# Performance work log

Hardware: AMD Instinct MI355X
Metric: run time of the kernel (lower is better)

Reference implementation:

```python
import jax, jax.numpy as jnp
from jax import lax
import numpy as np

C = 56; DI = 112; DS = 16; R = 4; K = 4; NB = 10; UP = 3
B, H, W = 1, 64, 64

def conv2d(x, w, b=None, pad=1, groups=1):
    out = lax.conv_general_dilated(x, w, (1, 1), [(pad, pad), (pad, pad)],
                                   feature_group_count=groups,
                                   dimension_numbers=('NCHW', 'OIHW', 'NCHW'))
    if b is not None:
        out = out + b[None, :, None, None]
    return out

def ln_last(x, w, b, eps=1e-5):
    mu = x.mean(-1, keepdims=True)
    var = ((x - mu) ** 2).mean(-1, keepdims=True)
    return (x - mu) / jnp.sqrt(var + eps) * w + b

def ln_cf(x, w, b, eps=1e-6):
    mu = x.mean(1, keepdims=True)
    var = ((x - mu) ** 2).mean(1, keepdims=True)
    return (x - mu) / jnp.sqrt(var + eps) * w[None, :, None, None] + b[None, :, None, None]

def bsconv(x, pw_w, dw_w, dw_b):
    x = conv2d(x, pw_w, pad=0)
    return conv2d(x, dw_w, dw_b, pad=1, groups=dw_w.shape[0])

def ss2d(x, p):
    # x: (B,H,W,C) -> SS2D (VMamba 4-direction selective scan)
    b, h, w, _ = x.shape
    L = h * w
    xz = x @ p['inproj_w'].T                        # (B,H,W,2*DI)
    xin, z = jnp.split(xz, 2, axis=-1)
    xc = jnp.transpose(xin, (0, 3, 1, 2))           # (B,DI,H,W)
    xc = jax.nn.silu(conv2d(xc, p['conv_w'], p['conv_b'], pad=1, groups=DI))
    xf = xc.reshape(b, DI, L)
    xt = jnp.swapaxes(xc, 2, 3).reshape(b, DI, L)
    x_hwwh = jnp.stack([xf, xt], axis=1)            # (B,2,DI,L)
    xs = jnp.concatenate([x_hwwh, jnp.flip(x_hwwh, -1)], axis=1)  # (B,K,DI,L)
    x_dbl = jnp.einsum('bkdl,kcd->bkcl', xs, p['xproj_w'])
    dts, Bs, Cs = jnp.split(x_dbl, [R, R + DS], axis=2)
    dts = jnp.einsum('bkrl,kdr->bkdl', dts, p['dt_w'])
    A = -jnp.exp(p['Alog'].reshape(K, DI, DS))
    delta = jax.nn.softplus(dts + p['dt_b'][None, :, :, None])    # (B,K,DI,L)

    def step(hst, inp):
        dl, xl, bl, cl = inp
        dA = jnp.exp(dl[..., None] * A[None])       # (B,K,DI,DS)
        hst = dA * hst + (dl * xl)[..., None] * bl[:, :, None, :]
        y = jnp.einsum('bkdn,bkn->bkd', hst, cl)
        return hst, y

    seq = (jnp.transpose(delta, (3, 0, 1, 2)), jnp.transpose(xs, (3, 0, 1, 2)),
           jnp.transpose(Bs, (3, 0, 1, 2)), jnp.transpose(Cs, (3, 0, 1, 2)))
    h0 = jnp.zeros((b, K, DI, DS), x.dtype)
    _, ys = lax.scan(step, h0, seq)                 # (L,B,K,DI)
    out_y = jnp.transpose(ys, (1, 2, 3, 0)) + p['D'].reshape(K, DI)[None, :, :, None] * xs
    inv = jnp.flip(out_y[:, 2:4], -1)
    y1 = out_y[:, 0]
    y2 = inv[:, 0]
    y3 = jnp.swapaxes(inv[:, 1].reshape(b, DI, w, h), 2, 3).reshape(b, DI, L)
    y4 = jnp.swapaxes(out_y[:, 1].reshape(b, DI, w, h), 2, 3).reshape(b, DI, L)
    y = jnp.swapaxes(y1 + y2 + y3 + y4, 1, 2).reshape(b, h, w, DI)
    y = ln_last(y, p['onorm_w'], p['onorm_b'])
    y = y * jax.nn.silu(z)
    return y @ p['outproj_w'].T

def safm(x, mfr_w, mfr_b, aggr_w, aggr_b):
    b, c, h, w = x.shape
    ch = c // 4
    parts = jnp.split(x, 4, axis=1)
    outs = []
    for i in range(4):
        s = parts[i]
        f = 2 ** i
        if i > 0:
            s = s.reshape(b, ch, h // f, f, w // f, f).max(axis=(3, 5))
        s = conv2d(s, mfr_w[i], mfr_b[i], pad=1, groups=ch)
        if i > 0:
            s = jnp.repeat(jnp.repeat(s, f, axis=2), f, axis=3)
        outs.append(s)
    out = conv2d(jnp.concatenate(outs, axis=1), aggr_w, aggr_b, pad=0)
    return jax.nn.gelu(out, approximate=False) * x

def afd(x, p):
    xn = jnp.transpose(x, (0, 2, 3, 1))
    xn = xn + ss2d(ln_last(xn, p['ln1_w'], p['ln1_b']), p)   # VSSBlock residual
    x = jnp.transpose(xn, (0, 3, 1, 2))
    x = x + safm(ln_cf(x, p['norm_w'], p['norm_b']), p['mfr_w'], p['mfr_b'], p['aggr_w'], p['aggr_b'])
    return x, x

def _forward(x, fea_pw_w, fea_dw_w, fea_dw_b,
             blk_ln1_w, blk_ln1_b, blk_inproj_w, blk_conv_w, blk_conv_b,
             blk_xproj_w, blk_dt_w, blk_dt_b, blk_Alog, blk_D,
             blk_onorm_w, blk_onorm_b, blk_outproj_w,
             blk_norm_w, blk_norm_b, blk_mfr_w, blk_mfr_b, blk_aggr_w, blk_aggr_b,
             c1_w, c1_b, norm_w, norm_b, c2_pw_w, c2_dw_w, c2_dw_b, up_w, up_b):
    out_fea = bsconv(x, fea_pw_w, fea_dw_w, fea_dw_b)
    bp = {'ln1_w': blk_ln1_w, 'ln1_b': blk_ln1_b, 'inproj_w': blk_inproj_w,
          'conv_w': blk_conv_w, 'conv_b': blk_conv_b, 'xproj_w': blk_xproj_w,
          'dt_w': blk_dt_w, 'dt_b': blk_dt_b, 'Alog': blk_Alog, 'D': blk_D,
          'onorm_w': blk_onorm_w, 'onorm_b': blk_onorm_b, 'outproj_w': blk_outproj_w,
          'norm_w': blk_norm_w, 'norm_b': blk_norm_b, 'mfr_w': blk_mfr_w,
          'mfr_b': blk_mfr_b, 'aggr_w': blk_aggr_w, 'aggr_b': blk_aggr_b}
    _, outs = lax.scan(afd, out_fea, bp)            # (NB,B,C,H,W) in B1..B10 order
    b, _, h, w = out_fea.shape
    trunk = jnp.transpose(outs, (1, 0, 2, 3, 4)).reshape(b, NB * C, h, w)
    out_B = conv2d(trunk, c1_w, c1_b, pad=0)
    out_B = jax.nn.gelu(ln_cf(out_B, norm_w, norm_b), approximate=False)
    out_lr = bsconv(out_B, c2_pw_w, c2_dw_w, c2_dw_b) + out_fea
    up = conv2d(out_lr, up_w, up_b, pad=1)          # (B, 3*UP*UP, H, W)
    oc = up.shape[1] // (UP * UP)
    ps = up.reshape(b, oc, UP, UP, h, w)
    return jnp.transpose(ps, (0, 1, 4, 2, 5, 3)).reshape(b, oc, h * UP, w * UP)

def setup_inputs():
    key = jax.random.key(0)
    ks = iter(jax.random.split(key, 40))
    rn = lambda shape, s=0.05: jax.random.normal(next(ks), shape, jnp.float32) * s
    ones = lambda shape: jnp.ones(shape, jnp.float32)
    zeros = lambda shape: jnp.zeros(shape, jnp.float32)
    return {
        'x': jax.random.normal(next(ks), (B, 3, H, W), jnp.float32),
        'fea_pw_w': rn((C, 3, 1, 1), 0.3),
        'fea_dw_w': rn((C, 1, 3, 3), 0.3),
        'fea_dw_b': zeros((C,)),
        'blk_ln1_w': ones((NB, C)), 'blk_ln1_b': zeros((NB, C)),
        'blk_inproj_w': rn((NB, 2 * DI, C)),
        'blk_conv_w': rn((NB, DI, 1, 3, 3), 0.2), 'blk_conv_b': zeros((NB, DI)),
        'blk_xproj_w': rn((NB, K, R + 2 * DS, DI)),
        'blk_dt_w': rn((NB, K, DI, R), 0.2),
        'blk_dt_b': jnp.full((NB, K, DI), -4.6, jnp.float32),
        'blk_Alog': jnp.broadcast_to(jnp.log(jnp.arange(1, DS + 1, dtype=jnp.float32)), (NB, K * DI, DS)) + jnp.zeros((NB, K * DI, DS), jnp.float32),
        'blk_D': ones((NB, K * DI)),
        'blk_onorm_w': ones((NB, DI)), 'blk_onorm_b': zeros((NB, DI)),
        'blk_outproj_w': rn((NB, C, DI)),
        'blk_norm_w': ones((NB, C)), 'blk_norm_b': zeros((NB, C)),
        'blk_mfr_w': rn((NB, 4, C // 4, 1, 3, 3), 0.2), 'blk_mfr_b': zeros((NB, 4, C // 4)),
        'blk_aggr_w': rn((NB, C, C, 1, 1)), 'blk_aggr_b': zeros((NB, C)),
        'c1_w': rn((C, NB * C, 1, 1)), 'c1_b': zeros((C,)),
        'norm_w': ones((C,)), 'norm_b': zeros((C,)),
        'c2_pw_w': rn((C, C, 1, 1)), 'c2_dw_w': rn((C, 1, 3, 3), 0.2), 'c2_dw_b': zeros((C,)),
        'up_w': rn((3 * UP * UP, C, 3, 3)), 'up_b': zeros((3 * UP * UP,)),
    }

def reference(x, fea_pw_w, fea_dw_w, fea_dw_b,
              blk_ln1_w, blk_ln1_b, blk_inproj_w, blk_conv_w, blk_conv_b,
              blk_xproj_w, blk_dt_w, blk_dt_b, blk_Alog, blk_D,
              blk_onorm_w, blk_onorm_b, blk_outproj_w,
              blk_norm_w, blk_norm_b, blk_mfr_w, blk_mfr_b, blk_aggr_w, blk_aggr_b,
              c1_w, c1_b, norm_w, norm_b, c2_pw_w, c2_dw_w, c2_dw_b, up_w, up_b):
    return _forward(x, fea_pw_w, fea_dw_w, fea_dw_b,
                    blk_ln1_w, blk_ln1_b, blk_inproj_w, blk_conv_w, blk_conv_b,
                    blk_xproj_w, blk_dt_w, blk_dt_b, blk_Alog, blk_D,
                    blk_onorm_w, blk_onorm_b, blk_outproj_w,
                    blk_norm_w, blk_norm_b, blk_mfr_w, blk_mfr_b, blk_aggr_w, blk_aggr_b,
                    c1_w, c1_b, norm_w, norm_b, c2_pw_w, c2_dw_w, c2_dw_b, up_w, up_b)
```

## Files before the change

kernel.cpp:

```cpp
#include <hip/hip_runtime.h>
#include <hip/hip_bf16.h>

#define HW 64
#define L4 4096
#define CC 56
#define DI 112
#define DSN 16
#define NBLK 10

typedef const float* BP;

__device__ __forceinline__ float bf(BP p, int i) { return p[i]; }
__device__ __forceinline__ float siluf(float x) { return x / (1.f + __expf(-x)); }
__device__ __forceinline__ float geluf(float x) { return 0.5f * x * (1.f + erff(x * 0.70710678f)); }

__global__ void k_fea_pw(BP x, BP w, float* __restrict__ t0) {
    int tid = blockIdx.x * blockDim.x + threadIdx.x;
    if (tid >= CC * L4) return;
    int c = tid >> 12, l = tid & 4095;
    float acc = 0.f;
    for (int i = 0; i < 3; ++i) acc += bf(x, i * L4 + l) * bf(w, c * 3 + i);
    t0[tid] = acc;
}

__global__ void __launch_bounds__(256) k_dw3x3t(
        const float* __restrict__ src, BP w, BP bvec, float* __restrict__ dst,
        int act, const float* __restrict__ addsrc) {
    int c = blockIdx.x >> 4;
    int tile = blockIdx.x & 15;
    int y0 = (tile >> 2) * 16, x0 = (tile & 3) * 16;
    __shared__ float sT[18 * 18];
    const float* sc = src + (size_t)c * L4;
    for (int idx = threadIdx.x; idx < 324; idx += 256) {
        int iy = idx / 18, ix = idx - iy * 18;
        int gy = y0 - 1 + iy, gx = x0 - 1 + ix;
        sT[idx] = (gy >= 0 && gy < 64 && gx >= 0 && gx < 64) ? sc[gy * 64 + gx] : 0.f;
    }
    __syncthreads();
    int py = threadIdx.x >> 4, px = threadIdx.x & 15;
    BP wr = w + c * 9;
    float acc = bvec ? bvec[c] : 0.f;
    #pragma unroll
    for (int ky = 0; ky < 3; ++ky)
        #pragma unroll
        for (int kx = 0; kx < 3; ++kx)
            acc += sT[(py + ky) * 18 + px + kx] * wr[ky * 3 + kx];
    if (act) acc = siluf(acc);
    int l = (y0 + py) * 64 + x0 + px;
    if (addsrc) acc += addsrc[(size_t)c * L4 + l];
    dst[(size_t)c * L4 + l] = acc;
}

__global__ void __launch_bounds__(256) k_ln56g(
        const float* __restrict__ part, BP bias, BP w, BP b, float* __restrict__ dst) {
    int lane = threadIdx.x & 63;
    int cg = threadIdx.x >> 6;
    int l0 = blockIdx.x * 64;
    __shared__ float sS[56 * 64];
    __shared__ float sPa[4][64], sPb[4][64];
    __shared__ float sMu[64], sRs[64];
    float ps = 0.f, ps2 = 0.f;
    for (int c = cg * 14; c < cg * 14 + 14; ++c) {
        float v = bias[c];
        #pragma unroll
        for (int z = 0; z < 5; ++z)
            v += part[(size_t)(z * 56 + c) * L4 + l0 + lane];
        sS[c * 64 + lane] = v; ps += v; ps2 += v * v;
    }
    sPa[cg][lane] = ps; sPb[cg][lane] = ps2;
    __syncthreads();
    if (threadIdx.x < 64) {
        float s = sPa[0][lane] + sPa[1][lane] + sPa[2][lane] + sPa[3][lane];
        float s2 = sPb[0][lane] + sPb[1][lane] + sPb[2][lane] + sPb[3][lane];
        float mu = s / 56.f;
        float var = fmaxf(s2 / 56.f - mu * mu, 0.f);
        sMu[lane] = mu; sRs[lane] = rsqrtf(var + 1e-6f);
    }
    __syncthreads();
    float mu = sMu[lane], rs = sRs[lane];
    for (int c = cg * 14; c < cg * 14 + 14; ++c) {
        float v = (sS[c * 64 + lane] - mu) * rs * w[c] + b[c];
        dst[(size_t)c * L4 + l0 + lane] = geluf(v);
    }
}

__global__ void __launch_bounds__(256) k_gemm(
        const float* __restrict__ src, BP w, BP bvec, const float* __restrict__ addsrc,
        float* __restrict__ dst, int nin, int nout) {
    int lane = threadIdx.x & 63;
    int jg = threadIdx.x >> 6;
    int l0 = blockIdx.x * 64;
    int j0 = blockIdx.y * 16;
    __shared__ __align__(16) float sS[56 * 64];
    __shared__ __align__(16) float sw[16 * 56];
    float acc[4] = {0.f, 0.f, 0.f, 0.f};

    for (int i0 = 0; i0 < nin; i0 += 56) {
        __syncthreads();
        for (int idx = threadIdx.x; idx < 56 * 64; idx += 256) {
            int ii = idx >> 6, px = idx & 63;
            sS[idx] = src[(size_t)(i0 + ii) * L4 + l0 + px];
        }
        for (int idx = threadIdx.x; idx < 16 * 56; idx += 256) {
            int jj = idx / 56, ii = idx - jj * 56;
            int j = j0 + jj;
            sw[idx] = (j < nout) ? w[(size_t)j * nin + i0 + ii] : 0.f;
        }
        __syncthreads();
        #pragma unroll
        for (int ii = 0; ii < 56; ii += 4) {
            float s0 = sS[(ii + 0) * 64 + lane];
            float s1 = sS[(ii + 1) * 64 + lane];
            float s2 = sS[(ii + 2) * 64 + lane];
            float s3 = sS[(ii + 3) * 64 + lane];
            #pragma unroll
            for (int jj = 0; jj < 4; ++jj) {
                const float4 wv = *(const float4*)&sw[(jg * 4 + jj) * 56 + ii];
                acc[jj] += s0 * wv.x + s1 * wv.y + s2 * wv.z + s3 * wv.w;
            }
        }
    }
    int l = l0 + lane;
    #pragma unroll
    for (int jj = 0; jj < 4; ++jj) {
        int j = j0 + jg * 4 + jj;
        if (j >= nout) continue;
        float v = acc[jj];
        if (bvec) v += bf(bvec, j);
        size_t idx = (size_t)j * L4 + l;
        if (addsrc) v += addsrc[idx];
        dst[idx] = v;
    }
}

__global__ void __launch_bounds__(256) k_c1(
        const float* __restrict__ src, BP w, float* __restrict__ part) {
    int lane = threadIdx.x & 63;
    int jg = threadIdx.x >> 6;
    int l0 = blockIdx.x * 64;
    int j0 = blockIdx.y * 16;
    int z = blockIdx.z;
    __shared__ __align__(16) float sS[56 * 64];
    __shared__ __align__(16) float sw[16 * 56];
    float acc[4] = {0.f, 0.f, 0.f, 0.f};

    for (int i0 = z * 112; i0 < z * 112 + 112; i0 += 56) {
        __syncthreads();
        for (int idx = threadIdx.x; idx < 56 * 64; idx += 256) {
            int ii = idx >> 6, px = idx & 63;
            sS[idx] = src[(size_t)(i0 + ii) * L4 + l0 + px];
        }
        for (int idx = threadIdx.x; idx < 16 * 56; idx += 256) {
            int jj = idx / 56, ii = idx - jj * 56;
            int j = j0 + jj;
            sw[idx] = (j < 56) ? w[(size_t)j * 560 + i0 + ii] : 0.f;
        }
        __syncthreads();
        #pragma unroll
        for (int ii = 0; ii < 56; ii += 4) {
            float s0 = sS[(ii + 0) * 64 + lane];
            float s1 = sS[(ii + 1) * 64 + lane];
            float s2 = sS[(ii + 2) * 64 + lane];
            float s3 = sS[(ii + 3) * 64 + lane];
            #pragma unroll
            for (int jj = 0; jj < 4; ++jj) {
                const float4 wv = *(const float4*)&sw[(jg * 4 + jj) * 56 + ii];
                acc[jj] += s0 * wv.x + s1 * wv.y + s2 * wv.z + s3 * wv.w;
            }
        }
    }
    int l = l0 + lane;
    #pragma unroll
    for (int jj = 0; jj < 4; ++jj) {
        int j = j0 + jg * 4 + jj;
        if (j < 56) part[(size_t)(z * 56 + j) * L4 + l] = acc[jj];
    }
}

__global__ void __launch_bounds__(256) k_xproj(
        const float* __restrict__ src, BP w, float* __restrict__ dst) {
    int lane = threadIdx.x & 31;
    int jg = threadIdx.x >> 5;
    int l0 = blockIdx.x * 32;
    int j0 = blockIdx.y * 16;
    __shared__ __align__(16) float sS[112 * 32];
    __shared__ __align__(16) float sw[16 * 112];
    float acc[2] = {0.f, 0.f};

    for (int idx = threadIdx.x; idx < 112 * 32; idx += 256) {
        int ii = idx >> 5, px = idx & 31;
        sS[idx] = src[(size_t)ii * L4 + l0 + px];
    }
    for (int idx = threadIdx.x; idx < 16 * 112; idx += 256) {
        int jj = idx / 112, ii = idx - jj * 112;
        sw[idx] = w[(size_t)(j0 + jj) * 112 + ii];
    }
    __syncthreads();
    #pragma unroll
    for (int ii = 0; ii < 112; ii += 4) {
        float s0 = sS[(ii + 0) * 32 + lane];
        float s1 = sS[(ii + 1) * 32 + lane];
        float s2 = sS[(ii + 2) * 32 + lane];
        float s3 = sS[(ii + 3) * 32 + lane];
        #pragma unroll
        for (int jj = 0; jj < 2; ++jj) {
            const float4 wv = *(const float4*)&sw[(jg * 2 + jj) * 112 + ii];
            acc[jj] += s0 * wv.x + s1 * wv.y + s2 * wv.z + s3 * wv.w;
        }
    }
    __syncthreads();
    #pragma unroll
    for (int jj = 0; jj < 2; ++jj)
        sS[(jg * 2 + jj) * 32 + lane] = acc[jj];
    __syncthreads();
    for (int idx = threadIdx.x; idx < 16 * 32; idx += 256) {
        int cidx = idx & 15, l2 = idx >> 4;
        int j = j0 + cidx;
        int k = j / 36, c = j - k * 36;
        dst[((size_t)k * L4 + l0 + l2) * 36 + c] = sS[cidx * 32 + l2];
    }
}

__global__ void __launch_bounds__(256) k_gemm_ln(
        const float* __restrict__ src, BP lnw, BP lnb, BP w,
        float* __restrict__ dst, int nout) {
    int lane = threadIdx.x & 63;
    int jg = threadIdx.x >> 6;
    int l0 = blockIdx.x * 64;
    int j0 = blockIdx.y * 16;
    __shared__ __align__(16) float sS[56 * 64];
    __shared__ __align__(16) float sw[16 * 56];
    __shared__ float sLw[56], sLb[56];
    float acc[4] = {0.f, 0.f, 0.f, 0.f};

    for (int idx = threadIdx.x; idx < 56 * 64; idx += 256) {
        int ii = idx >> 6, px = idx & 63;
        sS[idx] = src[(size_t)ii * L4 + l0 + px];
    }
    for (int idx = threadIdx.x; idx < 16 * 56; idx += 256) {
        int jj = idx / 56, ii = idx - jj * 56;
        int j = j0 + jj;
        sw[idx] = (j < nout) ? w[(size_t)j * 56 + ii] : 0.f;
    }
    if (threadIdx.x < 56) { sLw[threadIdx.x] = lnw[threadIdx.x]; sLb[threadIdx.x] = lnb[threadIdx.x]; }
    __syncthreads();
    if (threadIdx.x < 64) {
        int px = threadIdx.x;
        float s = 0.f, s2 = 0.f;
        for (int ii = 0; ii < 56; ++ii) { float v = sS[ii * 64 + px]; s += v; s2 += v * v; }
        float mu = s / 56.f;
        float var = fmaxf(s2 / 56.f - mu * mu, 0.f);
        float rstd = rsqrtf(var + 1e-5f);
        for (int ii = 0; ii < 56; ++ii)
            sS[ii * 64 + px] = (sS[ii * 64 + px] - mu) * rstd * sLw[ii] + sLb[ii];
    }
    __syncthreads();
    #pragma unroll
    for (int ii = 0; ii < 56; ii += 4) {
        float s0 = sS[(ii + 0) * 64 + lane];
        float s1 = sS[(ii + 1) * 64 + lane];
        float s2 = sS[(ii + 2) * 64 + lane];
        float s3 = sS[(ii + 3) * 64 + lane];
        #pragma unroll
        for (int jj = 0; jj < 4; ++jj) {
            const float4 wv = *(const float4*)&sw[(jg * 4 + jj) * 56 + ii];
            acc[jj] += s0 * wv.x + s1 * wv.y + s2 * wv.z + s3 * wv.w;
        }
    }
    int l = l0 + lane;
    #pragma unroll
    for (int jj = 0; jj < 4; ++jj) {
        int j = j0 + jg * 4 + jj;
        if (j < nout) dst[(size_t)j * L4 + l] = acc[jj];
    }
}

#define SPAD(p) ((p) + ((p) >> 5))
__global__ void __launch_bounds__(256) k_scan(
        const float* __restrict__ xc, const float* __restrict__ pk,
        BP Alog, BP dtw, BP dtb, float* __restrict__ ybuf) {
    int pair = blockIdx.x;
    int s = threadIdx.x & 3;
    int c = threadIdx.x >> 2;
    int k = pair / DI, d = pair - k * DI;
    const float4 al = *(const float4*)(Alog + pair * DSN + s * 4);
    float a0 = -__expf(al.x), a1 = -__expf(al.y), a2 = -__expf(al.z), a3 = -__expf(al.w);
    const float4 wdt = *(const float4*)(dtw + pair * 4);
    float db = dtb[pair];
    const float* xptr = xc + (size_t)d * L4;
    const float* pkk = pk + (size_t)k * L4 * 36;
    float* yptr = ybuf + (size_t)pair * L4;

    __shared__ float sDl[4224];
    __shared__ float sDlx[4224];
    __shared__ float sP[64 * 16];
    __shared__ float sHe[64 * 16];

    for (int p = threadIdx.x; p < L4; p += 256) {
        const float4 r4 = *(const float4*)(pkk + (size_t)p * 36);
        float v = db + r4.x * wdt.x + r4.y * wdt.y + r4.z * wdt.z + r4.w * wdt.w;
        float dl = fmaxf(v, 0.f) + __logf(1.f + __expf(-fabsf(v)));
        sDl[SPAD(p)] = dl;
        sDlx[SPAD(p)] = dl * xptr[p];
    }
    __syncthreads();

    int p0, dp;
    if (k == 0)      { p0 = c * 64;        dp = 1;   }
    else if (k == 1) { p0 = c;             dp = 64;  }
    else if (k == 2) { p0 = 4095 - c * 64; dp = -1;  }
    else             { p0 = 4095 - c;      dp = -64; }
    long rstep = (long)dp * 36;

    float h0 = 0.f, h1 = 0.f, h2 = 0.f, h3 = 0.f;
    float P0 = 1.f, P1 = 1.f, P2 = 1.f, P3 = 1.f;
    {
        int p = p0;
        const float* rB = pkk + (size_t)p0 * 36 + 4 + s * 4;
        for (int jb = 0; jb < 64; jb += 4) {
            float4 Bv[4]; float dlv[4], dxv[4];
            #pragma unroll
            for (int u = 0; u < 4; ++u) {
                Bv[u] = *(const float4*)(rB + u * rstep);
                int q = SPAD(p + u * dp);
                dlv[u] = sDl[q]; dxv[u] = sDlx[q];
            }
            #pragma unroll
            for (int u = 0; u < 4; ++u) {
                float e0 = __expf(dlv[u] * a0), e1 = __expf(dlv[u] * a1);
                float e2 = __expf(dlv[u] * a2), e3 = __expf(dlv[u] * a3);
                h0 = e0 * h0 + dxv[u] * Bv[u].x; P0 *= e0;
                h1 = e1 * h1 + dxv[u] * Bv[u].y; P1 *= e1;
                h2 = e2 * h2 + dxv[u] * Bv[u].z; P2 *= e2;
                h3 = e3 * h3 + dxv[u] * Bv[u].w; P3 *= e3;
            }
            p += 4 * dp; rB += 4 * rstep;
        }
    }
    int base = c * 16 + s * 4;
    sP[base + 0] = P0; sHe[base + 0] = h0;
    sP[base + 1] = P1; sHe[base + 1] = h1;
    sP[base + 2] = P2; sHe[base + 2] = h2;
    sP[base + 3] = P3; sHe[base + 3] = h3;
    __syncthreads();

    for (int off = 1; off < 64; off <<= 1) {
        float pC[4], hC[4], pL[4] = {0.f,0.f,0.f,0.f}, hL[4] = {0.f,0.f,0.f,0.f};
        #pragma unroll
        for (int u = 0; u < 4; ++u) { pC[u] = sP[base + u]; hC[u] = sHe[base + u]; }
        if (c >= off) {
            #pragma unroll
            for (int u = 0; u < 4; ++u) { pL[u] = sP[base - off * 16 + u]; hL[u] = sHe[base - off * 16 + u]; }
        }
        __syncthreads();
        if (c >= off) {
            #pragma unroll
            for (int u = 0; u < 4; ++u) { sP[base + u] = pC[u] * pL[u]; sHe[base + u] = pC[u] * hL[u] + hC[u]; }
        }
        __syncthreads();
    }

    if (c > 0) {
        h0 = sHe[base - 16 + 0]; h1 = sHe[base - 16 + 1];
        h2 = sHe[base - 16 + 2]; h3 = sHe[base - 16 + 3];
    } else { h0 = h1 = h2 = h3 = 0.f; }
    {
        int p = p0;
        const float* rB = pkk + (size_t)p0 * 36 + 4 + s * 4;
        const float* rC = pkk + (size_t)p0 * 36 + 20 + s * 4;
        for (int jb = 0; jb < 64; jb += 4) {
            float4 Bv[4], Cv[4]; float dlv[4], dxv[4];
            #pragma unroll
            for (int u = 0; u < 4; ++u) {
                Bv[u] = *(const float4*)(rB + u * rstep);
                Cv[u] = *(const float4*)(rC + u * rstep);
                int q = SPAD(p + u * dp);
                dlv[u] = sDl[q]; dxv[u] = sDlx[q];
            }
            #pragma unroll
            for (int u = 0; u < 4; ++u) {
                float e0 = __expf(dlv[u] * a0), e1 = __expf(dlv[u] * a1);
                float e2 = __expf(dlv[u] * a2), e3 = __expf(dlv[u] * a3);
                h0 = e0 * h0 + dxv[u] * Bv[u].x;
                h1 = e1 * h1 + dxv[u] * Bv[u].y;
                h2 = e2 * h2 + dxv[u] * Bv[u].z;
                h3 = e3 * h3 + dxv[u] * Bv[u].w;
                float y = h0 * Cv[u].x + h1 * Cv[u].y + h2 * Cv[u].z + h3 * Cv[u].w;
                y += __shfl_xor(y, 1, 4);
                y += __shfl_xor(y, 2, 4);
                if (s == 0) yptr[p + u * dp] = y;
            }
            p += 4 * dp; rB += 4 * rstep; rC += 4 * rstep;
        }
    }
}

__global__ void __launch_bounds__(256) k_comb_proj(
        const float* __restrict__ ybuf, const float* __restrict__ xc,
        const float* __restrict__ zbuf, BP Dp, BP ow, BP ob, BP opw,
        const float* __restrict__ xin, BP nw, BP nbv,
        float* __restrict__ x_mid, float* __restrict__ xln) {
    int lane = threadIdx.x & 15;
    int grp = threadIdx.x >> 4;
    int l0 = blockIdx.x * 16;
    __shared__ __align__(16) float sY[112 * 16];
    __shared__ __align__(16) float sW[56 * 112];
    __shared__ float sPa[16][16], sPb[16][16];
    __shared__ float sMu[16], sRs[16];

    float ps = 0.f, ps2 = 0.f;
    for (int d = grp * 7; d < grp * 7 + 7; ++d) {
        float Ds = Dp[d] + Dp[DI + d] + Dp[2 * DI + d] + Dp[3 * DI + d];
        float v = ybuf[(size_t)d * L4 + l0 + lane]
                + ybuf[(size_t)(DI + d) * L4 + l0 + lane]
                + ybuf[(size_t)(2 * DI + d) * L4 + l0 + lane]
                + ybuf[(size_t)(3 * DI + d) * L4 + l0 + lane]
                + Ds * xc[(size_t)d * L4 + l0 + lane];
        sY[d * 16 + lane] = v; ps += v; ps2 += v * v;
    }
    sPa[grp][lane] = ps; sPb[grp][lane] = ps2;
    for (int idx = threadIdx.x; idx < 56 * 112; idx += 256) sW[idx] = opw[idx];
    __syncthreads();
    if (threadIdx.x < 16) {
        float s = 0.f, s2 = 0.f;
        for (int g = 0; g < 16; ++g) { s += sPa[g][lane]; s2 += sPb[g][lane]; }
        float mu = s / 112.f;
        float var = fmaxf(s2 / 112.f - mu * mu, 0.f);
        sMu[lane] = mu; sRs[lane] = rsqrtf(var + 1e-5f);
    }
    __syncthreads();
    {
        float mu = sMu[lane], rs = sRs[lane];
        for (int d = grp * 7; d < grp * 7 + 7; ++d) {
            float v = (sY[d * 16 + lane] - mu) * rs * ow[d] + ob[d];
            float z = zbuf[(size_t)d * L4 + l0 + lane];
            sY[d * 16 + lane] = v * siluf(z);
        }
    }
    __syncthreads();

    float acc[4] = {0.f, 0.f, 0.f, 0.f};
    #pragma unroll 2
    for (int ii = 0; ii < 112; ii += 4) {
        float s0 = sY[(ii + 0) * 16 + lane];
        float s1 = sY[(ii + 1) * 16 + lane];
        float s2 = sY[(ii + 2) * 16 + lane];
        float s3 = sY[(ii + 3) * 16 + lane];
        #pragma unroll
        for (int jj = 0; jj < 4; ++jj) {
            int j = grp * 4 + jj;
            if (j < 56) {
                const float4 wv = *(const float4*)&sW[j * 112 + ii];
                acc[jj] += s0 * wv.x + s1 * wv.y + s2 * wv.z + s3 * wv.w;
            }
        }
    }
    int l = l0 + lane;
    float vout[4];
    float ps3 = 0.f, ps4 = 0.f;
    #pragma unroll
    for (int jj = 0; jj < 4; ++jj) {
        int j = grp * 4 + jj;
        vout[jj] = 0.f;
        if (j < 56) {
            float v = acc[jj] + xin[(size_t)j * L4 + l];
            vout[jj] = v;
            x_mid[(size_t)j * L4 + l] = v;
            ps3 += v; ps4 += v * v;
        }
    }
    __syncthreads();
    sPa[grp][lane] = ps3; sPb[grp][lane] = ps4;
    __syncthreads();
    if (threadIdx.x < 16) {
        float s = 0.f, s2 = 0.f;
        for (int g = 0; g < 16; ++g) { s += sPa[g][lane]; s2 += sPb[g][lane]; }
        float mu = s / 56.f;
        float var = fmaxf(s2 / 56.f - mu * mu, 0.f);
        sMu[lane] = mu; sRs[lane] = rsqrtf(var + 1e-6f);
    }
    __syncthreads();
    {
        float mu = sMu[lane], rs = sRs[lane];
        #pragma unroll
        for (int jj = 0; jj < 4; ++jj) {
            int j = grp * 4 + jj;
            if (j < 56) xln[(size_t)j * L4 + l] = (vout[jj] - mu) * rs * nw[j] + nbv[j];
        }
    }
}

__global__ void __launch_bounds__(256) k_safm(
        const float* __restrict__ xln, BP mw, BP mb,
        float* __restrict__ s0, float* __restrict__ s1,
        float* __restrict__ s2, float* __restrict__ s3) {
    int b = blockIdx.x;
    if (b < 224) {
        int c = b >> 4;
        int tile = b & 15;
        int y0 = (tile >> 2) * 16, x0 = (tile & 3) * 16;
        __shared__ float sT[18 * 18];
        const float* sc = xln + (size_t)c * L4;
        for (int idx = threadIdx.x; idx < 324; idx += 256) {
            int iy = idx / 18, ix = idx - iy * 18;
            int gy = y0 - 1 + iy, gx = x0 - 1 + ix;
            sT[idx] = (gy >= 0 && gy < 64 && gx >= 0 && gx < 64) ? sc[gy * 64 + gx] : 0.f;
        }
        __syncthreads();
        int py = threadIdx.x >> 4, px = threadIdx.x & 15;
        BP wr = mw + c * 9;
        float acc = mb[c];
        #pragma unroll
        for (int ky = 0; ky < 3; ++ky)
            #pragma unroll
            for (int kx = 0; kx < 3; ++kx)
                acc += sT[(py + ky) * 18 + px + kx] * wr[ky * 3 + kx];
        s0[c * L4 + (y0 + py) * 64 + x0 + px] = acc;
    } else {
        int bb = b - 224;
        int i = bb / 14 + 1;
        int c = bb % 14;
        int S = 64 >> i;
        int f = 1 << i;
        __shared__ float sP[34 * 34];
        int W2 = S + 2;
        for (int idx = threadIdx.x; idx < W2 * W2; idx += 256) sP[idx] = 0.f;
        __syncthreads();
        const float* sc = xln + (size_t)(i * 14 + c) * L4;
        for (int cell = threadIdx.x; cell < S * S; cell += 256) {
            int y = cell / S, x = cell - y * S;
            float m = -3.4e38f;
            for (int dy = 0; dy < f; ++dy)
                for (int dx = 0; dx < f; ++dx)
                    m = fmaxf(m, sc[(y * f + dy) * 64 + x * f + dx]);
            sP[(y + 1) * W2 + x + 1] = m;
        }
        __syncthreads();
        BP wr = mw + (i * 14 + c) * 9;
        float bias = mb[i * 14 + c];
        float* dst = (i == 1) ? s1 : (i == 2) ? s2 : s3;
        for (int cell = threadIdx.x; cell < S * S; cell += 256) {
            int y = cell / S, x = cell - y * S;
            float acc = bias;
            #pragma unroll
            for (int ky = 0; ky < 3; ++ky)
                #pragma unroll
                for (int kx = 0; kx < 3; ++kx)
                    acc += sP[(y + ky) * W2 + x + kx] * wr[ky * 3 + kx];
            dst[c * S * S + cell] = acc;
        }
    }
}

__global__ void k_aggr(const float* __restrict__ s0, const float* __restrict__ s1,
                       const float* __restrict__ s2, const float* __restrict__ s3,
                       const float* __restrict__ xln, const float* __restrict__ x_mid,
                       BP aw, BP ab, float* __restrict__ out) {
    int tid = blockIdx.x * blockDim.x + threadIdx.x;
    if (tid >= CC * L4) return;
    int c = tid >> 12, l = tid & 4095;
    int h = l >> 6, w = l & 63;
    int o1 = (h >> 1) * 32 + (w >> 1);
    int o2 = (h >> 2) * 16 + (w >> 2);
    int o3 = (h >> 3) * 8 + (w >> 3);
    float acc = bf(ab, c);
    BP wr = aw + c * 56;
    for (int cg = 0; cg < 14; ++cg) acc += s0[cg * 4096 + l]  * bf(wr, cg);
    for (int cg = 0; cg < 14; ++cg) acc += s1[cg * 1024 + o1] * bf(wr, 14 + cg);
    for (int cg = 0; cg < 14; ++cg) acc += s2[cg * 256 + o2]  * bf(wr, 28 + cg);
    for (int cg = 0; cg < 14; ++cg) acc += s3[cg * 64 + o3]   * bf(wr, 42 + cg);
    out[tid] = x_mid[tid] + geluf(acc) * xln[tid];
}

__global__ void __launch_bounds__(256) k_up(
        const float* __restrict__ out_lr, BP uw, BP ub, float* __restrict__ out) {
    __shared__ float sIn[56 * 36];
    __shared__ float sW[27 * 56 * 9];
    int b = blockIdx.x;
    int y0 = (b >> 4) * 4, x0 = (b & 15) * 4;
    for (int idx = threadIdx.x; idx < 56 * 36; idx += 256) {
        int cc = idx / 36; int rem = idx - cc * 36; int iy = rem / 6, ix = rem - iy * 6;
        int gy = y0 - 1 + iy, gx = x0 - 1 + ix;
        sIn[idx] = (gy >= 0 && gy < 64 && gx >= 0 && gx < 64)
                 ? out_lr[(size_t)cc * L4 + gy * 64 + gx] : 0.f;
    }
    for (int idx = threadIdx.x; idx < 27 * 56 * 9; idx += 256) sW[idx] = uw[idx];
    __syncthreads();
    int px = threadIdx.x & 15;
    int og = threadIdx.x >> 4;
    int dy = px >> 2, dx = px & 3;
    for (int oo = 0; oo < 2; ++oo) {
        int o = og * 2 + oo;
        if (o >= 27) break;
        float acc = ub[o];
        const float* wb = &sW[o * 504];
        for (int cc = 0; cc < 56; ++cc) {
            const float* ib = &sIn[cc * 36 + dy * 6 + dx];
            const float* wc = wb + cc * 9;
            acc += ib[0] * wc[0] + ib[1] * wc[1] + ib[2] * wc[2]
                 + ib[6] * wc[3] + ib[7] * wc[4] + ib[8] * wc[5]
                 + ib[12] * wc[6] + ib[13] * wc[7] + ib[14] * wc[8];
        }
        int h = y0 + dy, wv = x0 + dx;
        int ch = o / 9, rr = (o % 9) / 3, ss = o % 3;
        out[ch * 36864 + (h * 3 + rr) * 192 + (wv * 3 + ss)] = acc;
    }
}

extern "C" void kernel_launch(void* const* d_in, const int* in_sizes, int n_in,
                              void* d_out, int out_size, void* d_ws, size_t ws_size,
                              hipStream_t stream) {
    BP in0  = (BP)d_in[0];
    BP in1  = (BP)d_in[1];
    BP in2  = (BP)d_in[2];
    BP in3  = (BP)d_in[3];
    BP in4  = (BP)d_in[4];
    BP in5  = (BP)d_in[5];
    BP in6  = (BP)d_in[6];
    BP in7  = (BP)d_in[7];
    BP in8  = (BP)d_in[8];
    BP in9  = (BP)d_in[9];
    BP in10 = (BP)d_in[10];
    BP in11 = (BP)d_in[11];
    BP in12 = (BP)d_in[12];
    BP in13 = (BP)d_in[13];
    BP in14 = (BP)d_in[14];
    BP in15 = (BP)d_in[15];
    BP in16 = (BP)d_in[16];
    BP in17 = (BP)d_in[17];
    BP in18 = (BP)d_in[18];
    BP in19 = (BP)d_in[19];
    BP in20 = (BP)d_in[20];
    BP in21 = (BP)d_in[21];
    BP in22 = (BP)d_in[22];
    BP in23 = (BP)d_in[23];
    BP in24 = (BP)d_in[24];
    BP in25 = (BP)d_in[25];
    BP in26 = (BP)d_in[26];
    BP in27 = (BP)d_in[27];
    BP in28 = (BP)d_in[28];
    BP in29 = (BP)d_in[29];
    BP in30 = (BP)d_in[30];
    BP in31 = (BP)d_in[31];

    float* ws = (float*)d_ws;
    float* trunk   = ws; ws += 560 * L4;
    float* out_fea = ws; ws += CC * L4;
    float* t0      = ws; ws += CC * L4;
    float* xz      = ws; ws += 224 * L4;
    float* xc      = ws; ws += DI * L4;
    float* pk      = ws; ws += 4 * 36 * L4;
    float* ybuf    = ws; ws += 4 * DI * L4;
    float* x_mid   = ws; ws += CC * L4;
    float* xln     = ws; ws += CC * L4;
    float* s0      = ws; ws += 14 * 4096;
    float* s1      = ws; ws += 14 * 1024;
    float* s2      = ws; ws += 14 * 256;
    float* s3      = ws; ws += 14 * 64;
    float* part    = ws; ws += 5 * 56 * L4;
    float* gB      = ws; ws += CC * L4;
    float* tbuf    = ws; ws += CC * L4;
    float* out_lr  = ws; ws += CC * L4;

    auto nb256 = [](int n) { return dim3((n + 255) / 256); };
    auto gemm_grid = [](int nout) { return dim3(64, (nout + 15) / 16); };

    k_fea_pw<<<nb256(CC * L4), 256, 0, stream>>>(in0, in1, t0);
    k_dw3x3t<<<dim3(CC * 16), 256, 0, stream>>>(t0, in2, in3, out_fea, 0, nullptr);

    for (int nb = 0; nb < NBLK; ++nb) {
        const float* xin = (nb == 0) ? out_fea : trunk + (size_t)(nb - 1) * CC * L4;
        float* xout = trunk + (size_t)nb * CC * L4;
        BP ln1w = in4 + nb * 56,        ln1b = in5 + nb * 56;
        BP ipw  = in6 + nb * 224 * 56;
        BP cw   = in7 + nb * 112 * 9,   cb   = in8 + nb * 112;
        BP xpw  = in9 + nb * 4 * 36 * 112;
        BP dtw  = in10 + nb * 4 * 112 * 4, dtb = in11 + nb * 448;
        BP alog = in12 + nb * 448 * 16, Dp   = in13 + nb * 448;
        BP onw  = in14 + nb * 112,      onb  = in15 + nb * 112;
        BP opw  = in16 + nb * 56 * 112;
        BP nw   = in17 + nb * 56,       nbv  = in18 + nb * 56;
        BP mw   = in19 + nb * 4 * 14 * 9, mb = in20 + nb * 56;
        BP aw   = in21 + nb * 56 * 56,  ab   = in22 + nb * 56;

        k_gemm_ln<<<gemm_grid(224), 256, 0, stream>>>(xin, ln1w, ln1b, ipw, xz, 224);
        k_dw3x3t<<<dim3(DI * 16), 256, 0, stream>>>(xz, cw, cb, xc, 1, nullptr);
        k_xproj<<<dim3(128, 9), 256, 0, stream>>>(xc, xpw, pk);
        k_scan<<<dim3(4 * DI), 256, 0, stream>>>(xc, pk, alog, dtw, dtb, ybuf);
        k_comb_proj<<<dim3(256), 256, 0, stream>>>(ybuf, xc, xz + 112 * L4, Dp, onw, onb, opw,
                                                   xin, nw, nbv, x_mid, xln);
        k_safm<<<dim3(266), 256, 0, stream>>>(xln, mw, mb, s0, s1, s2, s3);
        k_aggr<<<nb256(CC * L4), 256, 0, stream>>>(s0, s1, s2, s3, xln, x_mid, aw, ab, xout);
    }

    k_c1<<<dim3(64, 4, 5), 256, 0, stream>>>(trunk, in23, part);
    k_ln56g<<<dim3(64), 256, 0, stream>>>(part, in24, in25, in26, gB);
    k_gemm<<<gemm_grid(56), 256, 0, stream>>>(gB, in27, nullptr, nullptr, tbuf, 56, 56);
    k_dw3x3t<<<dim3(CC * 16), 256, 0, stream>>>(tbuf, in28, in29, out_lr, 0, out_fea);
    k_up<<<dim3(256), 256, 0, stream>>>(out_lr, in30, in31, (float*)d_out);
}
```

Before: 1.158 ms.

## Split scan into 128 chunks per sequence and fuse stem pointwise into depthwise conv

The selective scan block now uses 512 threads, so each sequence is cut into 128 chunks of 32 steps instead of 64 chunks of 64. This halves the serial per-thread recurrence and raises parallelism, at the cost of one more prefix-combine level and doubled shared scratch for the carry arrays. Separately, the 3-channel pointwise stem conv is fused into the depthwise 3x3 kernel's halo load, removing one launch and an intermediate buffer round trip.

```diff
diff --git a/kernel.cpp b/kernel.cpp
--- a/kernel.cpp
+++ b/kernel.cpp
@@ -14,13 +14,33 @@
 __device__ __forceinline__ float siluf(float x) { return x / (1.f + __expf(-x)); }
 __device__ __forceinline__ float geluf(float x) { return 0.5f * x * (1.f + erff(x * 0.70710678f)); }
 
-__global__ void k_fea_pw(BP x, BP w, float* __restrict__ t0) {
-    int tid = blockIdx.x * blockDim.x + threadIdx.x;
-    if (tid >= CC * L4) return;
-    int c = tid >> 12, l = tid & 4095;
-    float acc = 0.f;
-    for (int i = 0; i < 3; ++i) acc += bf(x, i * L4 + l) * bf(w, c * 3 + i);
-    t0[tid] = acc;
+__global__ void __launch_bounds__(256) k_stem(
+        BP x, BP pw, BP dw, BP db, float* __restrict__ dst) {
+    int c = blockIdx.x >> 4;
+    int tile = blockIdx.x & 15;
+    int y0 = (tile >> 2) * 16, x0 = (tile & 3) * 16;
+    __shared__ float sT[18 * 18];
+    float w0 = pw[c * 3], w1 = pw[c * 3 + 1], w2 = pw[c * 3 + 2];
+    for (int idx = threadIdx.x; idx < 324; idx += 256) {
+        int iy = idx / 18, ix = idx - iy * 18;
+        int gy = y0 - 1 + iy, gx = x0 - 1 + ix;
+        float v = 0.f;
+        if (gy >= 0 && gy < 64 && gx >= 0 && gx < 64) {
+            int g = gy * 64 + gx;
+            v = w0 * x[g] + w1 * x[L4 + g] + w2 * x[2 * L4 + g];
+        }
+        sT[idx] = v;
+    }
+    __syncthreads();
+    int py = threadIdx.x >> 4, px = threadIdx.x & 15;
+    BP wr = dw + c * 9;
+    float acc = db[c];
+    #pragma unroll
+    for (int ky = 0; ky < 3; ++ky)
+        #pragma unroll
+        for (int kx = 0; kx < 3; ++kx)
+            acc += sT[(py + ky) * 18 + px + kx] * wr[ky * 3 + kx];
+    dst[(size_t)c * L4 + (y0 + py) * 64 + x0 + px] = acc;
 }
 
 __global__ void __launch_bounds__(256) k_dw3x3t(
@@ -276,7 +296,7 @@
 }
 
 #define SPAD(p) ((p) + ((p) >> 5))
-__global__ void __launch_bounds__(256) k_scan(
+__global__ void __launch_bounds__(512) k_scan(
         const float* __restrict__ xc, const float* __restrict__ pk,
         BP Alog, BP dtw, BP dtb, float* __restrict__ ybuf) {
     int pair = blockIdx.x;
@@ -293,10 +313,10 @@
 
     __shared__ float sDl[4224];
     __shared__ float sDlx[4224];
-    __shared__ float sP[64 * 16];
-    __shared__ float sHe[64 * 16];
-
-    for (int p = threadIdx.x; p < L4; p += 256) {
+    __shared__ float sP[128 * 16];
+    __shared__ float sHe[128 * 16];
+
+    for (int p = threadIdx.x; p < L4; p += 512) {
         const float4 r4 = *(const float4*)(pkk + (size_t)p * 36);
         float v = db + r4.x * wdt.x + r4.y * wdt.y + r4.z * wdt.z + r4.w * wdt.w;
         float dl = fmaxf(v, 0.f) + __logf(1.f + __expf(-fabsf(v)));
@@ -306,10 +326,10 @@
     __syncthreads();
 
     int p0, dp;
-    if (k == 0)      { p0 = c * 64;        dp = 1;   }
-    else if (k == 1) { p0 = c;             dp = 64;  }
-    else if (k == 2) { p0 = 4095 - c * 64; dp = -1;  }
-    else             { p0 = 4095 - c;      dp = -64; }
+    if (k == 0)      { p0 = c * 32;                              dp = 1;   }
+    else if (k == 1) { p0 = (c & 1) * 2048 + (c >> 1);           dp = 64;  }
+    else if (k == 2) { p0 = 4095 - c * 32;                       dp = -1;  }
+    else             { p0 = 4095 - ((c & 1) * 2048 + (c >> 1));  dp = -64; }
     long rstep = (long)dp * 36;
 
     float h0 = 0.f, h1 = 0.f, h2 = 0.f, h3 = 0.f;
@@ -317,7 +337,7 @@
     {
         int p = p0;
         const float* rB = pkk + (size_t)p0 * 36 + 4 + s * 4;
-        for (int jb = 0; jb < 64; jb += 4) {
+        for (int jb = 0; jb < 32; jb += 4) {
             float4 Bv[4]; float dlv[4], dxv[4];
             #pragma unroll
             for (int u = 0; u < 4; ++u) {
@@ -344,7 +364,7 @@
     sP[base + 3] = P3; sHe[base + 3] = h3;
     __syncthreads();
 
-    for (int off = 1; off < 64; off <<= 1) {
+    for (int off = 1; off < 128; off <<= 1) {
         float pC[4], hC[4], pL[4] = {0.f,0.f,0.f,0.f}, hL[4] = {0.f,0.f,0.f,0.f};
         #pragma unroll
         for (int u = 0; u < 4; ++u) { pC[u] = sP[base + u]; hC[u] = sHe[base + u]; }
@@ -368,7 +388,7 @@
         int p = p0;
         const float* rB = pkk + (size_t)p0 * 36 + 4 + s * 4;
         const float* rC = pkk + (size_t)p0 * 36 + 20 + s * 4;
-        for (int jb = 0; jb < 64; jb += 4) {
+        for (int jb = 0; jb < 32; jb += 4) {
             float4 Bv[4], Cv[4]; float dlv[4], dxv[4];
             #pragma unroll
             for (int u = 0; u < 4; ++u) {
@@ -646,7 +666,6 @@
     float* ws = (float*)d_ws;
     float* trunk   = ws; ws += 560 * L4;
     float* out_fea = ws; ws += CC * L4;
-    float* t0      = ws; ws += CC * L4;
     float* xz      = ws; ws += 224 * L4;
     float* xc      = ws; ws += DI * L4;
     float* pk      = ws; ws += 4 * 36 * L4;
@@ -665,8 +684,7 @@
     auto nb256 = [](int n) { return dim3((n + 255) / 256); };
     auto gemm_grid = [](int nout) { return dim3(64, (nout + 15) / 16); };
 
-    k_fea_pw<<<nb256(CC * L4), 256, 0, stream>>>(in0, in1, t0);
-    k_dw3x3t<<<dim3(CC * 16), 256, 0, stream>>>(t0, in2, in3, out_fea, 0, nullptr);
+    k_stem<<<dim3(CC * 16), 256, 0, stream>>>(in0, in1, in2, in3, out_fea);
 
     for (int nb = 0; nb < NBLK; ++nb) {
         const float* xin = (nb == 0) ? out_fea : trunk + (size_t)(nb - 1) * CC * L4;
@@ -686,7 +704,7 @@
         k_gemm_ln<<<gemm_grid(224), 256, 0, stream>>>(xin, ln1w, ln1b, ipw, xz, 224);
         k_dw3x3t<<<dim3(DI * 16), 256, 0, stream>>>(xz, cw, cb, xc, 1, nullptr);
         k_xproj<<<dim3(128, 9), 256, 0, stream>>>(xc, xpw, pk);
-        k_scan<<<dim3(4 * DI), 256, 0, stream>>>(xc, pk, alog, dtw, dtb, ybuf);
+        k_scan<<<dim3(4 * DI), 512, 0, stream>>>(xc, pk, alog, dtw, dtb, ybuf);
         k_comb_proj<<<dim3(256), 256, 0, stream>>>(ybuf, xc, xz + 112 * L4, Dp, onw, onb, opw,
                                                    xin, nw, nbv, x_mid, xln);
         k_safm<<<dim3(266), 256, 0, stream>>>(xln, mw, mb, s0, s1, s2, s3);
```

Result: slower. 1.197 ms (+3.4%).
